# Kernel tuning notes

Hardware: AMD Instinct MI355X
Metric: run time of the kernel (lower is better)

## Reference

```python
import jax, jax.numpy as jnp
import numpy as np

NUM_HEADS = 8

def setup_inputs() -> dict:
    key = jax.random.key(0)
    ks = jax.random.split(key, 7)
    B, H, W, C = 4, 56, 56, 256
    Nq = 1
    std = 0.02
    return {
        "x": jax.random.normal(ks[0], (B, H, W, C), jnp.float32),
        "cls_token": jax.random.normal(ks[1], (B, Nq, C), jnp.float32),
        "qkv_w": jax.random.normal(ks[2], (3 * C, C), jnp.float32) * std,
        "proj_w": jax.random.normal(ks[3], (C, C), jnp.float32) * std,
        "proj_b": jnp.zeros((C,), jnp.float32),
        "lepe_w": jax.random.normal(ks[4], (C, 1, 5, 5), jnp.float32) * std,
        "lepe_b": jnp.zeros((C,), jnp.float32),
    }

def reference(x, cls_token, qkv_w, proj_w, proj_b, lepe_w, lepe_b):
    B, H, W, C = x.shape
    N = H * W
    Nq = cls_token.shape[1]
    hd = C // NUM_HEADS
    scale = hd ** -0.5

    x_seq = x.reshape(B, N, C)
    x_cat = jnp.concatenate([cls_token, x_seq], axis=1)        # [B, Nq+N, C]

    qkv = x_cat @ qkv_w.T                                      # [B, Nq+N, 3C]
    qkv = qkv.reshape(B, Nq + N, 3, NUM_HEADS, hd)
    q, k, v = qkv[:, :, 0], qkv[:, :, 1], qkv[:, :, 2]         # [B, S, h, d]

    attn = jnp.einsum('bshd,bthd->bhst', q, k) * scale         # [B, h, S, S]
    attn = jax.nn.softmax(attn, axis=-1)
    out = jnp.einsum('bhst,bthd->bshd', attn, v).reshape(B, Nq + N, C)

    cls_out, x_out = out[:, :Nq], out[:, Nq:]

    # depthwise conv LePE on the raw spatial input
    x_nchw = jnp.transpose(x, (0, 3, 1, 2))                    # [B, C, H, W]
    lepe = jax.lax.conv_general_dilated(
        x_nchw, lepe_w, window_strides=(1, 1), padding='SAME',
        feature_group_count=C,
        dimension_numbers=('NCHW', 'OIHW', 'NCHW'))
    lepe = lepe + lepe_b[None, :, None, None]
    lepe = jnp.transpose(lepe, (0, 2, 3, 1)).reshape(B, N, C)

    x_out = (x_out + lepe) @ proj_w.T + proj_b
    cls_out = cls_out @ proj_w.T + proj_b
    return x_out.reshape(B, H, W, C), cls_out
```

## Files before the change

### kernel.cpp

```cpp
#include <hip/hip_runtime.h>
#include <math.h>

#define BB 4
#define HH 56
#define WW 56
#define CC 256
#define NN 3136
#define SS 3137
#define NH 8
#define HD 32
#define M_ROWS (BB * SS)
#define SPAD 3200
#define QSCALE (0.17677669529663687f * 1.4426950408889634f)
#define KT 128

typedef short short8 __attribute__((ext_vector_type(8)));
typedef short bf4    __attribute__((ext_vector_type(4)));
typedef float f32x4  __attribute__((ext_vector_type(4)));

static __device__ __forceinline__ unsigned short f2bf(float f) {
    union { float f; unsigned u; } a; a.f = f;
    unsigned r = a.u + 0x7FFF + ((a.u >> 16) & 1);
    return (unsigned short)(r >> 16);
}
static __device__ __forceinline__ float bf2f(unsigned short h) {
    union { unsigned u; float f; } a; a.u = ((unsigned)h) << 16; return a.f;
}

__global__ __launch_bounds__(256)
void pre(const float* __restrict__ x, const float* __restrict__ cls,
         const float* __restrict__ qkv_w, const float* __restrict__ proj_w,
         const float* __restrict__ lepe_w,
         unsigned short* __restrict__ xb, unsigned short* __restrict__ wb,
         unsigned short* __restrict__ pwhi, unsigned short* __restrict__ pwlo,
         unsigned short* __restrict__ vt, float* __restrict__ wt,
         unsigned short* __restrict__ lepe)
{
    const int B0 = 3137;
    const int B1 = B0 + 192;
    const int B2 = B1 + 64;
    const int B3 = B2 + 64;
    const int B4 = B3 + 25;
    int blk = blockIdx.x, tid = threadIdx.x;
    if (blk < B0) {
        int row = blk * 4 + (tid >> 6);
        int c0 = (tid & 63) * 4;
        int b = row / SS, s = row % SS;
        const float* src = (s == 0) ? (cls + (size_t)b * CC)
                                    : (x + ((size_t)b * NN + (s - 1)) * CC);
        float4 v = *(const float4*)(src + c0);
        bf4 pk;
        pk[0] = (short)f2bf(v.x); pk[1] = (short)f2bf(v.y);
        pk[2] = (short)f2bf(v.z); pk[3] = (short)f2bf(v.w);
        *(bf4*)(xb + (size_t)row * CC + c0) = pk;
    } else if (blk < B1) {
        int row = (blk - B0) * 4 + (tid >> 6);
        int c0 = (tid & 63) * 4;
        float4 v = *(const float4*)(qkv_w + (size_t)row * CC + c0);
        bf4 pk;
        pk[0] = (short)f2bf(v.x); pk[1] = (short)f2bf(v.y);
        pk[2] = (short)f2bf(v.z); pk[3] = (short)f2bf(v.w);
        *(bf4*)(wb + (size_t)row * CC + c0) = pk;
    } else if (blk < B2) {
        int row = (blk - B1) * 4 + (tid >> 6);
        int c0 = (tid & 63) * 4;
        float4 v = *(const float4*)(proj_w + (size_t)row * CC + c0);
        bf4 ph, pl;
        float vv[4] = {v.x, v.y, v.z, v.w};
        #pragma unroll
        for (int e = 0; e < 4; ++e) {
            unsigned short h = f2bf(vv[e]);
            ph[e] = (short)h;
            pl[e] = (short)f2bf(vv[e] - bf2f(h));
        }
        *(bf4*)(pwhi + (size_t)row * CC + c0) = ph;
        *(bf4*)(pwlo + (size_t)row * CC + c0) = pl;
    } else if (blk < B3) {
        int idx = blk - B2;
        int row = idx * 16 + (tid >> 4);
        int col = 3136 + (tid & 15) * 4;
        bf4 z = {};
        *(bf4*)(vt + (size_t)row * SPAD + col) = z;
    } else if (blk < B4) {
        int t = blk - B3;
        wt[(size_t)t * CC + tid] = lepe_w[(size_t)tid * 25 + t];
    } else {
        int b = blk - B4;
        lepe[((size_t)b * SS) * CC + tid] = 0;
    }
}

__global__ __launch_bounds__(256)
void lepe_tiled(const unsigned short* __restrict__ xb,
                const float* __restrict__ wt, const float* __restrict__ bias,
                unsigned short* __restrict__ lepe)
{
    __shared__ unsigned short Xs[144][72];
    __shared__ float Wls[25][68];

    const int tid = threadIdx.x;
    const int bid = blockIdx.x;
    const int sp  = bid % 49;
    const int ct  = (bid / 49) & 3;
    const int b   = bid / 196;
    const int y0 = (sp / 7) * 8, x0 = (sp % 7) * 8;
    const int c0 = ct * 64;

    const int cq = tid & 15;
    const int pg = tid >> 4;

    #pragma unroll
    for (int r = 0; r < 9; ++r) {
        int seg = r * 16 + pg;
        int dy = seg / 12, dx = seg % 12;
        int yy = y0 + dy - 2, xc = x0 + dx - 2;
        bf4 v = {};
        if (yy >= 0 && yy < HH && xc >= 0 && xc < WW)
            v = *(const bf4*)(xb + ((size_t)(b * SS + 1 + yy * WW + xc)) * CC + c0 + cq * 4);
        *(bf4*)&Xs[seg][cq * 4] = v;
    }
    for (int idx = tid; idx < 1600; idx += 256) {
        int t = idx >> 6, c = idx & 63;
        Wls[t][c] = wt[(size_t)t * CC + c0 + c];
    }
    __syncthreads();

    float4 bq = *(const float4*)(bias + c0 + cq * 4);
    f32x4 acc[4];
    #pragma unroll
    for (int it = 0; it < 4; ++it) {
        acc[it][0] = bq.x; acc[it][1] = bq.y; acc[it][2] = bq.z; acc[it][3] = bq.w;
    }
    int hbase[4];
    #pragma unroll
    for (int it = 0; it < 4; ++it) {
        int pos = it * 16 + pg;
        hbase[it] = (pos >> 3) * 12 + (pos & 7);
    }

    #pragma unroll
    for (int t = 0; t < 25; ++t) {
        int dy = t / 5, dx = t % 5;
        float4 wq = *(const float4*)&Wls[t][cq * 4];
        #pragma unroll
        for (int it = 0; it < 4; ++it) {
            const unsigned short* xp = &Xs[hbase[it] + dy * 12 + dx][cq * 4];
            uint2 dv = *(const uint2*)xp;
            float e0 = __uint_as_float(dv.x << 16);
            float e1 = __uint_as_float(dv.x & 0xFFFF0000u);
            float e2 = __uint_as_float(dv.y << 16);
            float e3 = __uint_as_float(dv.y & 0xFFFF0000u);
            acc[it][0] += e0 * wq.x; acc[it][1] += e1 * wq.y;
            acc[it][2] += e2 * wq.z; acc[it][3] += e3 * wq.w;
        }
    }

    #pragma unroll
    for (int it = 0; it < 4; ++it) {
        int pos = it * 16 + pg;
        int py = pos >> 3, px = pos & 7;
        bf4 pk;
        pk[0] = (short)f2bf(acc[it][0]); pk[1] = (short)f2bf(acc[it][1]);
        pk[2] = (short)f2bf(acc[it][2]); pk[3] = (short)f2bf(acc[it][3]);
        *(bf4*)(lepe + ((size_t)(b * SS + 1 + (y0 + py) * WW + (x0 + px))) * CC
                + c0 + cq * 4) = pk;
    }
}

__global__ __launch_bounds__(256)
void qkv_mfma(const unsigned short* __restrict__ xb,
              const unsigned short* __restrict__ wb,
              unsigned short* __restrict__ qb, unsigned short* __restrict__ kb,
              unsigned short* __restrict__ vt)
{
    __shared__ unsigned short As[64][76];
    __shared__ unsigned short Bs[128][76];
    const int tid = threadIdx.x;
    const int w = tid >> 6, lane = tid & 63, lo = lane & 15, hi = lane >> 4;
    const int b0 = blockIdx.x / 50;
    const int s0blk = (blockIdx.x % 50) * 64;
    const int col0 = blockIdx.y * 128;
    const int wm = (w & 1) * 32, wn = (w >> 1) * 64;

    f32x4 acc[2][4] = {};

    const int arow = tid >> 3, ac8 = (tid & 7) * 8;
    const int brow = tid >> 3, bc8 = (tid & 7) * 8;

    short8 avr[2], bvr[4];
    #pragma unroll
    for (int i = 0; i < 2; ++i) {
        int row = arow + i * 32;
        short8 av = {};
        if (s0blk + row < SS)
            av = *(const short8*)(xb + (size_t)(b0 * SS + s0blk + row) * CC + ac8);
        avr[i] = av;
    }
    #pragma unroll
    for (int i = 0; i < 4; ++i)
        bvr[i] = *(const short8*)(wb + (size_t)(col0 + brow + i * 32) * CC + bc8);

    for (int k0 = 0; k0 < CC; k0 += 64) {
        __syncthreads();
        #pragma unroll
        for (int i = 0; i < 2; ++i)
            *(short8*)&As[arow + i * 32][ac8] = avr[i];
        #pragma unroll
        for (int i = 0; i < 4; ++i)
            *(short8*)&Bs[brow + i * 32][bc8] = bvr[i];
        __syncthreads();

        int kn = k0 + 64;
        if (kn < CC) {
            #pragma unroll
            for (int i = 0; i < 2; ++i) {
                int row = arow + i * 32;
                short8 av = {};
                if (s0blk + row < SS)
                    av = *(const short8*)(xb + (size_t)(b0 * SS + s0blk + row) * CC + kn + ac8);
                avr[i] = av;
            }
            #pragma unroll
            for (int i = 0; i < 4; ++i)
                bvr[i] = *(const short8*)(wb + (size_t)(col0 + brow + i * 32) * CC + kn + bc8);
        }

        #pragma unroll
        for (int kk = 0; kk < 64; kk += 32) {
            short8 af[2], bf_[4];
            #pragma unroll
            for (int m = 0; m < 2; ++m)
                af[m] = *(const short8*)&As[wm + m * 16 + lo][kk + hi * 8];
            #pragma unroll
            for (int n = 0; n < 4; ++n)
                bf_[n] = *(const short8*)&Bs[wn + n * 16 + lo][kk + hi * 8];
            #pragma unroll
            for (int m = 0; m < 2; ++m)
                #pragma unroll
                for (int n = 0; n < 4; ++n)
                    acc[m][n] = __builtin_amdgcn_mfma_f32_16x16x32_bf16(
                                    af[m], bf_[n], acc[m][n], 0, 0, 0);
        }
    }

    const int part = col0 >> 8;
    if (part < 2) {
        #pragma unroll
        for (int m = 0; m < 2; ++m) {
            #pragma unroll
            for (int rr = 0; rr < 4; ++rr) {
                int s = s0blk + wm + m * 16 + hi * 4 + rr;
                if (s >= SS) continue;
                size_t r = (size_t)(b0 * SS + s);
                #pragma unroll
                for (int n = 0; n < 4; ++n) {
                    int cc = (col0 + wn + n * 16 + lo) & 255;
                    float val = acc[m][n][rr];
                    if (part == 0) qb[r * CC + cc] = f2bf(val * QSCALE);
                    else           kb[r * CC + cc] = f2bf(val);
                }
            }
        }
    } else {
        #pragma unroll
        for (int m = 0; m < 2; ++m) {
            int s0 = s0blk + wm + m * 16 + hi * 4;
            if (s0 >= SS) continue;
            bool fast = (s0 + 3 < SS);
            #pragma unroll
            for (int n = 0; n < 4; ++n) {
                int cc = (col0 + wn + n * 16 + lo) & 255;
                int hh = cc >> 5, d = cc & 31;
                unsigned short* vrow = vt + (size_t)((b0 * NH + hh) * HD + d) * SPAD;
                if (fast) {
                    bf4 pk;
                    pk[0] = (short)f2bf(acc[m][n][0]);
                    pk[1] = (short)f2bf(acc[m][n][1]);
                    pk[2] = (short)f2bf(acc[m][n][2]);
                    pk[3] = (short)f2bf(acc[m][n][3]);
                    *(bf4*)(vrow + s0) = pk;
                } else {
                    for (int rr = 0; rr < 4 && s0 + rr < SS; ++rr)
                        vrow[s0 + rr] = f2bf(acc[m][n][rr]);
                }
            }
        }
    }
}

__global__ __launch_bounds__(256)
void attn_mfma(const unsigned short* __restrict__ qb,
               const unsigned short* __restrict__ kb,
               const unsigned short* __restrict__ vt,
               const unsigned short* __restrict__ lepe,
               unsigned short* __restrict__ ohi)
{
    __shared__ unsigned short Ks[KT][44];
    __shared__ unsigned short Vts[32][140];

    const int tid  = threadIdx.x;
    const int lane = tid & 63;
    const int w    = tid >> 6;
    const int lo   = lane & 15;
    const int hi   = lane >> 4;

    const int bid = blockIdx.x;
    const int h   = bid & 7;
    const int j   = bid >> 3;
    const int qc  = j % 50;
    const int b   = j / 50;
    const int q0w = qc * 64 + w * 16;

    const int qrow = min(q0w + lo, SS - 1);
    const short8 qa = *(const short8*)(qb + ((size_t)(b * SS + qrow)) * CC + h * HD + hi * 8);

    f32x4 oacc[2] = {};
    f32x4 dacc = {};
    bf4 ones;
    ones[0] = (short)0x3F80; ones[1] = (short)0x3F80;
    ones[2] = (short)0x3F80; ones[3] = (short)0x3F80;

    const int krow = tid >> 2, kd0 = (tid & 3) * 8;
    const int vrow = tid >> 4, vk0 = (tid & 15) * 8;
    const unsigned short* kp0 = kb + ((size_t)b * SS + krow) * CC + h * HD + kd0;
    const unsigned short* vp0 = vt + ((size_t)((b * NH + h) * HD + vrow)) * SPAD + vk0;

    short8 kv0 = *(const short8*)(kp0);
    short8 kv1 = *(const short8*)(kp0 + (size_t)64 * CC);
    short8 vv0 = *(const short8*)(vp0);
    short8 vv1 = *(const short8*)(vp0 + (size_t)16 * SPAD);

    for (int k0 = 0; k0 < SPAD; k0 += KT) {
        __syncthreads();
        *(short8*)&Ks[krow][kd0]       = kv0;
        *(short8*)&Ks[64 + krow][kd0]  = kv1;
        *(short8*)&Vts[vrow][vk0]      = vv0;
        *(short8*)&Vts[16 + vrow][vk0] = vv1;
        __syncthreads();

        int kn = k0 + KT;
        if (kn < SPAD) {
            short8 z = {};
            kv0 = (kn + krow < SS)      ? *(const short8*)(kp0 + (size_t)kn * CC)        : z;
            kv1 = (kn + 64 + krow < SS) ? *(const short8*)(kp0 + (size_t)(kn + 64) * CC) : z;
            vv0 = *(const short8*)(vp0 + kn);
            vv1 = *(const short8*)(vp0 + (size_t)16 * SPAD + kn);
        }

        #pragma unroll
        for (int g = 0; g < 8; ++g) {
            short8 kf = *(const short8*)&Ks[g * 16 + lo][hi * 8];
            bf4 vf0 = *(const bf4*)&Vts[lo][g * 16 + hi * 4];
            bf4 vf1 = *(const bf4*)&Vts[16 + lo][g * 16 + hi * 4];
            f32x4 st = __builtin_amdgcn_mfma_f32_16x16x32_bf16(
                           kf, qa, (f32x4){0.f, 0.f, 0.f, 0.f}, 0, 0, 0);
            float p0 = __builtin_amdgcn_exp2f(st[0]);
            float p1 = __builtin_amdgcn_exp2f(st[1]);
            float p2 = __builtin_amdgcn_exp2f(st[2]);
            float p3 = __builtin_amdgcn_exp2f(st[3]);
            unsigned u01 = __builtin_amdgcn_perm(
                __float_as_uint(p1), __float_as_uint(p0), 0x07060302u);
            unsigned u23 = __builtin_amdgcn_perm(
                __float_as_uint(p3), __float_as_uint(p2), 0x07060302u);
            union { unsigned u[2]; bf4 s; } pf;
            pf.u[0] = u01; pf.u[1] = u23;
            oacc[0] = __builtin_amdgcn_mfma_f32_16x16x16bf16_1k(vf0, pf.s, oacc[0], 0, 0, 0);
            oacc[1] = __builtin_amdgcn_mfma_f32_16x16x16bf16_1k(vf1, pf.s, oacc[1], 0, 0, 0);
            dacc    = __builtin_amdgcn_mfma_f32_16x16x16bf16_1k(ones, pf.s, dacc, 0, 0, 0);
        }
    }

    float inv = 1.f / (dacc[0] - 63.f);
    int rowq = q0w + lo;
    if (rowq < SS) {
        size_t base = ((size_t)(b * SS + rowq)) * CC + h * HD;
        #pragma unroll
        for (int dt = 0; dt < 2; ++dt) {
            bf4 lep = *(const bf4*)(lepe + base + dt * 16 + hi * 4);
            bf4 pk;
            #pragma unroll
            for (int r = 0; r < 4; ++r) {
                float val = oacc[dt][r] * inv + bf2f((unsigned short)lep[r]);
                pk[r] = (short)f2bf(val);
            }
            *(bf4*)(ohi + base + dt * 16 + hi * 4) = pk;
        }
    }
}

__global__ __launch_bounds__(256)
void proj_mfma(const unsigned short* __restrict__ ohi,
               const unsigned short* __restrict__ pwhi,
               const unsigned short* __restrict__ pwlo,
               const float* __restrict__ bias, float* __restrict__ out)
{
    __shared__ unsigned short Ah[64][76];
    __shared__ unsigned short Wh[64][76];
    __shared__ unsigned short Wl[64][76];
    const int tid = threadIdx.x;
    const int w = tid >> 6, lane = tid & 63, lo = lane & 15, hi = lane >> 4;
    const int row0 = blockIdx.x * 64, col0 = blockIdx.y * 64;
    const int wm = (w & 1) * 32, wn = (w >> 1) * 32;

    f32x4 acc[2][2] = {};

    const int srow = tid >> 3, sc8 = (tid & 7) * 8;

    short8 ar[2], whr[2], wlr[2];
    #pragma unroll
    for (int i = 0; i < 2; ++i) {
        int gr = row0 + srow + i * 32;
        short8 ah = {};
        if (gr < M_ROWS) ah = *(const short8*)(ohi + (size_t)gr * CC + sc8);
        ar[i] = ah;
        int wr = col0 + srow + i * 32;
        whr[i] = *(const short8*)(pwhi + (size_t)wr * CC + sc8);
        wlr[i] = *(const short8*)(pwlo + (size_t)wr * CC + sc8);
    }

    for (int k0 = 0; k0 < CC; k0 += 64) {
        __syncthreads();
        #pragma unroll
        for (int i = 0; i < 2; ++i) {
            *(short8*)&Ah[srow + i * 32][sc8] = ar[i];
            *(short8*)&Wh[srow + i * 32][sc8] = whr[i];
            *(short8*)&Wl[srow + i * 32][sc8] = wlr[i];
        }
        __syncthreads();

        int kn = k0 + 64;
        if (kn < CC) {
            #pragma unroll
            for (int i = 0; i < 2; ++i) {
                int gr = row0 + srow + i * 32;
                short8 ah = {};
                if (gr < M_ROWS) ah = *(const short8*)(ohi + (size_t)gr * CC + kn + sc8);
                ar[i] = ah;
                int wr = col0 + srow + i * 32;
                whr[i] = *(const short8*)(pwhi + (size_t)wr * CC + kn + sc8);
                wlr[i] = *(const short8*)(pwlo + (size_t)wr * CC + kn + sc8);
            }
        }

        #pragma unroll
        for (int kk = 0; kk < 64; kk += 32) {
            short8 ah[2], wh[2], wl[2];
            #pragma unroll
            for (int m = 0; m < 2; ++m)
                ah[m] = *(const short8*)&Ah[wm + m * 16 + lo][kk + hi * 8];
            #pragma unroll
            for (int n = 0; n < 2; ++n) {
                wh[n] = *(const short8*)&Wh[wn + n * 16 + lo][kk + hi * 8];
                wl[n] = *(const short8*)&Wl[wn + n * 16 + lo][kk + hi * 8];
            }
            #pragma unroll
            for (int m = 0; m < 2; ++m)
                #pragma unroll
                for (int n = 0; n < 2; ++n) {
                    acc[m][n] = __builtin_amdgcn_mfma_f32_16x16x32_bf16(
                                    ah[m], wh[n], acc[m][n], 0, 0, 0);
                    acc[m][n] = __builtin_amdgcn_mfma_f32_16x16x32_bf16(
                                    ah[m], wl[n], acc[m][n], 0, 0, 0);
                }
        }
    }

    #pragma unroll
    for (int m = 0; m < 2; ++m) {
        #pragma unroll
        for (int rr = 0; rr < 4; ++rr) {
            int r = row0 + wm + m * 16 + hi * 4 + rr;
            if (r >= M_ROWS) continue;
            int b = r / SS, s = r % SS;
            #pragma unroll
            for (int n = 0; n < 2; ++n) {
                int col = col0 + wn + n * 16 + lo;
                float val = acc[m][n][rr] + bias[col];
                if (s == 0)
                    out[(size_t)BB * NN * CC + (size_t)b * CC + col] = val;
                else
                    out[((size_t)b * NN + (s - 1)) * CC + col] = val;
            }
        }
    }
}

extern "C" void kernel_launch(void* const* d_in, const int* in_sizes, int n_in,
                              void* d_out, int out_size, void* d_ws, size_t ws_size,
                              hipStream_t stream)
{
    const float* x      = (const float*)d_in[0];
    const float* cls    = (const float*)d_in[1];
    const float* qkv_w  = (const float*)d_in[2];
    const float* proj_w = (const float*)d_in[3];
    const float* proj_b = (const float*)d_in[4];
    const float* lepe_w = (const float*)d_in[5];
    const float* lepe_b = (const float*)d_in[6];
    float* out = (float*)d_out;

    char* ws = (char*)d_ws;
    unsigned short* qb   = (unsigned short*)(ws + 0);
    unsigned short* kb   = (unsigned short*)(ws + 6424576);
    unsigned short* vt   = (unsigned short*)(ws + 12849152);
    unsigned short* xb   = (unsigned short*)(ws + 19402752);
    unsigned short* wb   = (unsigned short*)(ws + 25827328);
    unsigned short* lepe = (unsigned short*)(ws + 26220544);
    unsigned short* ohi  = (unsigned short*)(ws + 32645120);
    unsigned short* pwhi = (unsigned short*)(ws + 39069696);
    unsigned short* pwlo = (unsigned short*)(ws + 39200768);
    float*          wt   = (float*)(ws + 39331840);

    const int PRE_BLKS = 3137 + 192 + 64 + 64 + 25 + 4;
    pre       <<<PRE_BLKS, 256, 0, stream>>>(x, cls, qkv_w, proj_w, lepe_w,
                                             xb, wb, pwhi, pwlo, vt, wt, lepe);
    lepe_tiled<<<784, 256, 0, stream>>>(xb, wt, lepe_b, lepe);
    qkv_mfma  <<<dim3(200, 6), 256, 0, stream>>>(xb, wb, qb, kb, vt);
    attn_mfma <<<1600, 256, 0, stream>>>(qb, kb, vt, lepe, ohi);
    proj_mfma <<<dim3(197, 4), 256, 0, stream>>>(ohi, pwhi, pwlo, proj_b, out);
}
```

Measured before the change: 202.4 us.

## Process two query groups per wave in attention to reuse K/V tiles

Each wave in the attention kernel now handles 32 query rows (two 16-row groups) instead of 16, so a block covers 128 queries and the grid shrinks from 1600 to 800 blocks. Every K/V tile staged in shared memory, and every fragment read from it, now feeds twice as many MFMA score and PV products, which cuts global and LDS traffic per query. The cost is more accumulator registers per thread (possibly lower occupancy) and fewer blocks to spread across the CUs. A no-op rewrite of the px expression in the LePE kernel is also included.

```diff
diff --git a/kernel.cpp b/kernel.cpp
--- a/kernel.cpp
+++ b/kernel.cpp
@@ -158,7 +158,7 @@
     #pragma unroll
     for (int it = 0; it < 4; ++it) {
         int pos = it * 16 + pg;
-        int py = pos >> 3, px = pos & 7;
+        int py = pos >> 3, px = pos & 8 - 1 < 0 ? 0 : (pos & 7);
         bf4 pk;
         pk[0] = (short)f2bf(acc[it][0]); pk[1] = (short)f2bf(acc[it][1]);
         pk[2] = (short)f2bf(acc[it][2]); pk[3] = (short)f2bf(acc[it][3]);
@@ -307,15 +307,19 @@
     const int bid = blockIdx.x;
     const int h   = bid & 7;
     const int j   = bid >> 3;
-    const int qc  = j % 50;
-    const int b   = j / 50;
-    const int q0w = qc * 64 + w * 16;
-
-    const int qrow = min(q0w + lo, SS - 1);
-    const short8 qa = *(const short8*)(qb + ((size_t)(b * SS + qrow)) * CC + h * HD + hi * 8);
-
-    f32x4 oacc[2] = {};
-    f32x4 dacc = {};
+    const int qc  = j % 25;
+    const int b   = j / 25;
+    const int q0w = qc * 128 + w * 32;
+
+    short8 qa[2];
+    #pragma unroll
+    for (int qg = 0; qg < 2; ++qg) {
+        int row = min(q0w + qg * 16 + lo, SS - 1);
+        qa[qg] = *(const short8*)(qb + ((size_t)(b * SS + row)) * CC + h * HD + hi * 8);
+    }
+
+    f32x4 oacc[2][2] = {};
+    f32x4 dacc[2] = {};
     bf4 ones;
     ones[0] = (short)0x3F80; ones[1] = (short)0x3F80;
     ones[2] = (short)0x3F80; ones[3] = (short)0x3F80;
@@ -352,38 +356,47 @@
             short8 kf = *(const short8*)&Ks[g * 16 + lo][hi * 8];
             bf4 vf0 = *(const bf4*)&Vts[lo][g * 16 + hi * 4];
             bf4 vf1 = *(const bf4*)&Vts[16 + lo][g * 16 + hi * 4];
-            f32x4 st = __builtin_amdgcn_mfma_f32_16x16x32_bf16(
-                           kf, qa, (f32x4){0.f, 0.f, 0.f, 0.f}, 0, 0, 0);
-            float p0 = __builtin_amdgcn_exp2f(st[0]);
-            float p1 = __builtin_amdgcn_exp2f(st[1]);
-            float p2 = __builtin_amdgcn_exp2f(st[2]);
-            float p3 = __builtin_amdgcn_exp2f(st[3]);
-            unsigned u01 = __builtin_amdgcn_perm(
-                __float_as_uint(p1), __float_as_uint(p0), 0x07060302u);
-            unsigned u23 = __builtin_amdgcn_perm(
-                __float_as_uint(p3), __float_as_uint(p2), 0x07060302u);
-            union { unsigned u[2]; bf4 s; } pf;
-            pf.u[0] = u01; pf.u[1] = u23;
-            oacc[0] = __builtin_amdgcn_mfma_f32_16x16x16bf16_1k(vf0, pf.s, oacc[0], 0, 0, 0);
-            oacc[1] = __builtin_amdgcn_mfma_f32_16x16x16bf16_1k(vf1, pf.s, oacc[1], 0, 0, 0);
-            dacc    = __builtin_amdgcn_mfma_f32_16x16x16bf16_1k(ones, pf.s, dacc, 0, 0, 0);
-        }
-    }
-
-    float inv = 1.f / (dacc[0] - 63.f);
-    int rowq = q0w + lo;
-    if (rowq < SS) {
-        size_t base = ((size_t)(b * SS + rowq)) * CC + h * HD;
-        #pragma unroll
-        for (int dt = 0; dt < 2; ++dt) {
-            bf4 lep = *(const bf4*)(lepe + base + dt * 16 + hi * 4);
-            bf4 pk;
-            #pragma unroll
-            for (int r = 0; r < 4; ++r) {
-                float val = oacc[dt][r] * inv + bf2f((unsigned short)lep[r]);
-                pk[r] = (short)f2bf(val);
-            }
-            *(bf4*)(ohi + base + dt * 16 + hi * 4) = pk;
+            #pragma unroll
+            for (int qg = 0; qg < 2; ++qg) {
+                f32x4 st = __builtin_amdgcn_mfma_f32_16x16x32_bf16(
+                               kf, qa[qg], (f32x4){0.f, 0.f, 0.f, 0.f}, 0, 0, 0);
+                float p0 = __builtin_amdgcn_exp2f(st[0]);
+                float p1 = __builtin_amdgcn_exp2f(st[1]);
+                float p2 = __builtin_amdgcn_exp2f(st[2]);
+                float p3 = __builtin_amdgcn_exp2f(st[3]);
+                unsigned u01 = __builtin_amdgcn_perm(
+                    __float_as_uint(p1), __float_as_uint(p0), 0x07060302u);
+                unsigned u23 = __builtin_amdgcn_perm(
+                    __float_as_uint(p3), __float_as_uint(p2), 0x07060302u);
+                union { unsigned u[2]; bf4 s; } pf;
+                pf.u[0] = u01; pf.u[1] = u23;
+                oacc[qg][0] = __builtin_amdgcn_mfma_f32_16x16x16bf16_1k(
+                                  vf0, pf.s, oacc[qg][0], 0, 0, 0);
+                oacc[qg][1] = __builtin_amdgcn_mfma_f32_16x16x16bf16_1k(
+                                  vf1, pf.s, oacc[qg][1], 0, 0, 0);
+                dacc[qg]    = __builtin_amdgcn_mfma_f32_16x16x16bf16_1k(
+                                  ones, pf.s, dacc[qg], 0, 0, 0);
+            }
+        }
+    }
+
+    #pragma unroll
+    for (int qg = 0; qg < 2; ++qg) {
+        float inv = 1.f / (dacc[qg][0] - 63.f);
+        int rowq = q0w + qg * 16 + lo;
+        if (rowq < SS) {
+            size_t base = ((size_t)(b * SS + rowq)) * CC + h * HD;
+            #pragma unroll
+            for (int dt = 0; dt < 2; ++dt) {
+                bf4 lep = *(const bf4*)(lepe + base + dt * 16 + hi * 4);
+                bf4 pk;
+                #pragma unroll
+                for (int r = 0; r < 4; ++r) {
+                    float val = oacc[qg][dt][r] * inv + bf2f((unsigned short)lep[r]);
+                    pk[r] = (short)f2bf(val);
+                }
+                *(bf4*)(ohi + base + dt * 16 + hi * 4) = pk;
+            }
         }
     }
 }
@@ -515,6 +528,6 @@
                                              xb, wb, pwhi, pwlo, vt, wt, lepe);
     lepe_tiled<<<784, 256, 0, stream>>>(xb, wt, lepe_b, lepe);
     qkv_mfma  <<<dim3(200, 6), 256, 0, stream>>>(xb, wb, qb, kb, vt);
-    attn_mfma <<<1600, 256, 0, stream>>>(qb, kb, vt, lepe, ohi);
+    attn_mfma <<<800, 256, 0, stream>>>(qb, kb, vt, lepe, ohi);
     proj_mfma <<<dim3(197, 4), 256, 0, stream>>>(ohi, pwhi, pwlo, proj_b, out);
 }
```

Measured after the change: 193.5 us. -4.4%, faster.
